# Optimization experiments

Hardware: AMD Instinct MI355X
Metric: run time of the kernel (lower is better)

Reference implementation:

```python
import jax, jax.numpy as jnp
import numpy as np

DIM = 768
TIME_DIM = 768
NUM_HEADS = 12
NUM_PATCHES = 784
GRID = 28  # sqrt(NUM_PATCHES)
REL_MAX = 2 * GRID - 1  # 55


def _rel_pos_indices():
    # Faithful to the torch buffer: relative_position_index = (dh + g-1) + (dw + g-1)
    coords = np.stack(np.meshgrid(np.arange(GRID), np.arange(GRID), indexing='ij'))  # [2,g,g]
    cf = coords.reshape(2, -1)  # [2,N]
    rel = cf[:, :, None] - cf[:, None, :]  # [2,N,N]
    rel = rel.transpose(1, 2, 0)
    rel[:, :, 0] += GRID - 1
    rel[:, :, 1] += GRID - 1
    idx = rel.sum(-1)  # [N,N], values in [0, 2*(2g-2)]
    # forward then splits this summed index (as written in the source):
    ih = idx // REL_MAX
    iw = idx % REL_MAX
    return jnp.asarray(ih, jnp.int32), jnp.asarray(iw, jnp.int32)


def setup_inputs() -> dict:
    key = jax.random.key(0)
    ks = jax.random.split(key, 16)
    B = 8
    s = 0.02
    inp = {
        'x_s': jax.random.normal(ks[0], (B, NUM_PATCHES, DIM), jnp.float32),
        'x_t': jax.random.normal(ks[1], (B, TIME_DIM), jnp.float32),
        'Wqs': jax.random.normal(ks[2], (DIM, DIM), jnp.float32) * s,
        'Wqt': jax.random.normal(ks[3], (TIME_DIM, DIM), jnp.float32) * s,
        'Wks': jax.random.normal(ks[4], (DIM, DIM), jnp.float32) * s,
        'Wkt': jax.random.normal(ks[5], (TIME_DIM, DIM), jnp.float32) * s,
        'Wvs': jax.random.normal(ks[6], (DIM, DIM), jnp.float32) * s,
        'Wvt': jax.random.normal(ks[7], (TIME_DIM, DIM), jnp.float32) * s,
        'rpb_table': jax.random.normal(ks[8], (REL_MAX, REL_MAX, NUM_HEADS), jnp.float32) * s,
        'proj_w': jax.random.normal(ks[9], (DIM, DIM), jnp.float32) * s,
        'proj_b': jnp.zeros((DIM,), jnp.float32),
    }
    return inp


def reference(x_s, x_t, Wqs, Wqt, Wks, Wkt, Wvs, Wvt, rpb_table, proj_w, proj_b):
    B, N, D = x_s.shape
    H = NUM_HEADS
    hd = D // H
    scale = hd ** -0.5

    # time-embed fused QKV: q = x_s @ Wqs + x_t @ Wqt (broadcast over tokens)
    q = x_s @ Wqs + (x_t @ Wqt)[:, None, :]
    k = x_s @ Wks + (x_t @ Wkt)[:, None, :]
    v = x_s @ Wvs + (x_t @ Wvt)[:, None, :]

    q = q.reshape(B, N, H, hd).transpose(0, 2, 1, 3)  # [B,H,N,hd]
    k = k.reshape(B, N, H, hd).transpose(0, 2, 1, 3)
    v = v.reshape(B, N, H, hd).transpose(0, 2, 1, 3)

    attn = jnp.einsum('bhnd,bhmd->bhnm', q, k) * scale  # [B,H,N,N]

    ih, iw = _rel_pos_indices()  # [N,N] each
    bias = rpb_table[ih, iw]  # [N,N,H]
    attn = attn + bias.transpose(2, 0, 1)[None]  # [1,H,N,N]

    attn = jax.nn.softmax(attn, axis=-1)
    x = jnp.einsum('bhnm,bhmd->bhnd', attn, v)
    x = x.transpose(0, 2, 1, 3).reshape(B, N, D)
    return x @ proj_w + proj_b
```

## Files before the change

kernel.cpp:

```cpp
#include <hip/hip_runtime.h>
#include <hip/hip_bf16.h>
#include <stdint.h>

#define DIM 768
#define NP  784
#define NH  12
#define HD  64
#define BATCH 8
#define MROWS (BATCH*NP)
#define MPAD 832
#define NCHUNK 32
#define KCH 24
#define L2E 1.4426950408889634f

using bf16x8 = __attribute__((ext_vector_type(8))) short;
using bf16x4 = __attribute__((ext_vector_type(4))) short;
using f32x4  = __attribute__((ext_vector_type(4))) float;

__device__ __forceinline__ short f2bf(float f) {
  union { float f; uint32_t u; } c; c.f = f;
  uint32_t u = c.u;
  u += 0x7FFFu + ((u >> 16) & 1u);
  return (short)(u >> 16);
}

__device__ __forceinline__ short bfr(float x) {
  union { __hip_bfloat16 b; short s; } u;
  u.b = __float2bfloat16(x);
  return u.s;
}

__device__ __forceinline__ void gld_lds16(const void* g, void* l) {
  __builtin_amdgcn_global_load_lds((const __attribute__((address_space(1))) uint32_t*)g,
                                   (__attribute__((address_space(3))) uint32_t*)l,
                                   16, 0, 0);
}

__global__ __launch_bounds__(256) void cvt_bf16_kernel(const float* __restrict__ src,
                                                       short* __restrict__ dst, int n8) {
  int i = blockIdx.x * 256 + threadIdx.x;
  if (i >= n8) return;
  const float4* s = (const float4*)src;
  float4 a = s[2*i], b = s[2*i+1];
  bf16x8 o;
  o[0]=f2bf(a.x); o[1]=f2bf(a.y); o[2]=f2bf(a.z); o[3]=f2bf(a.w);
  o[4]=f2bf(b.x); o[5]=f2bf(b.y); o[6]=f2bf(b.z); o[7]=f2bf(b.w);
  ((bf16x8*)dst)[i] = o;
}

__global__ __launch_bounds__(256) void wtrans_kernel(const float* __restrict__ w0,
                                                     const float* __restrict__ w1,
                                                     const float* __restrict__ w2,
                                                     const float* __restrict__ w3,
                                                     short* __restrict__ dst) {
  __shared__ float tile[32][33];
  const int z = blockIdx.z;
  const float* src = (z==0) ? w0 : (z==1) ? w1 : (z==2) ? w2 : w3;
  short* d = dst + (size_t)z * DIM * DIM;
  const int n0 = blockIdx.x*32, k0 = blockIdx.y*32;
  const int tx = threadIdx.x, ty = threadIdx.y;
#pragma unroll
  for (int i=0;i<4;i++) tile[ty+i*8][tx] = src[(size_t)(k0+ty+i*8)*DIM + n0+tx];
  __syncthreads();
#pragma unroll
  for (int i=0;i<4;i++) d[(size_t)(n0+ty+i*8)*DIM + k0+tx] = f2bf(tile[tx][ty+i*8]);
}

__global__ __launch_bounds__(256) void tvec1_kernel(const float* __restrict__ x_t,
                                                    const float* __restrict__ wq,
                                                    const float* __restrict__ wk,
                                                    const float* __restrict__ wv,
                                                    float* __restrict__ part) {
  const int z = blockIdx.x, kc = blockIdx.y;
  const float* w = (z==0) ? wq : (z==1) ? wk : wv;
  const int d = threadIdx.x;
  __shared__ float xs[BATCH][KCH];
  if (threadIdx.x < BATCH*KCH)
    xs[threadIdx.x / KCH][threadIdx.x % KCH] =
        x_t[(size_t)(threadIdx.x / KCH)*DIM + kc*KCH + threadIdx.x % KCH];
  __syncthreads();
  float a0[BATCH] = {}, a1[BATCH] = {}, a2[BATCH] = {};
#pragma unroll 4
  for (int k = 0; k < KCH; ++k) {
    const float* wr = w + (size_t)(kc*KCH + k)*DIM + d;
    float w0 = wr[0], w1 = wr[256], w2 = wr[512];
#pragma unroll
    for (int b = 0; b < BATCH; ++b) {
      float xv = xs[b][k];
      a0[b] += xv*w0; a1[b] += xv*w1; a2[b] += xv*w2;
    }
  }
#pragma unroll
  for (int b = 0; b < BATCH; ++b) {
    float* p = part + (((size_t)z*NCHUNK + kc)*BATCH + b)*DIM + d;
    p[0] = a0[b]; p[256] = a1[b]; p[512] = a2[b];
  }
}

__global__ __launch_bounds__(256) void tvec2_kernel(const float* __restrict__ part,
                                                    float* __restrict__ t) {
  const int i = blockIdx.x*256 + threadIdx.x;
  if (i >= 3*BATCH*DIM) return;
  const int z = i / (BATCH*DIM), rem = i % (BATCH*DIM);
  float s = 0.f;
#pragma unroll 8
  for (int c = 0; c < NCHUNK; ++c)
    s += part[((size_t)z*NCHUNK + c)*BATCH*DIM + rem];
  t[i] = s;
}

template<int MODE>
__global__ __launch_bounds__(256) void gemm_kernel(const short* __restrict__ A,
                                                   const short* __restrict__ Bw,
                                                   const float* __restrict__ aux,
                                                   short* __restrict__ outq,
                                                   short* __restrict__ outk,
                                                   short* __restrict__ outv,
                                                   float* __restrict__ outf) {
  __shared__ short As[128*32];
  __shared__ short Bs[128*32];
  const int bx = blockIdx.x, by = blockIdx.y, z = blockIdx.z;
  const short* Bz = Bw + (size_t)z * DIM * DIM;
  const int tid = threadIdx.x, w = tid>>6, lane = tid&63;
  const int wr = w>>1, wc = w&1, ln15 = lane&15, lg = lane>>4;
  const int m0 = by*128, n0 = bx*128;

  f32x4 acc[4][4] = {};

  for (int kt=0; kt<24; ++kt) {
    const int k0 = kt*32;
    __syncthreads();
#pragma unroll
    for (int i=0;i<2;i++) {
      const int inst = w*2 + i;
      const int off  = inst*1024 + lane*16;
      const int row  = off >> 6;
      const int ce   = (off & 63) >> 1;
      gld_lds16(A  + (size_t)(m0+row)*DIM + k0 + ce, (char*)As + (size_t)inst*1024);
      gld_lds16(Bz + (size_t)(n0+row)*DIM + k0 + ce, (char*)Bs + (size_t)inst*1024);
    }
    __syncthreads();
    bf16x8 af[4], bfr_[4];
#pragma unroll
    for (int mi=0;mi<4;mi++) af[mi]   = *(const bf16x8*)&As[(wr*64+mi*16+ln15)*32 + lg*8];
#pragma unroll
    for (int ni=0;ni<4;ni++) bfr_[ni] = *(const bf16x8*)&Bs[(wc*64+ni*16+ln15)*32 + lg*8];
#pragma unroll
    for (int mi=0;mi<4;mi++)
#pragma unroll
      for (int ni=0;ni<4;ni++)
        acc[mi][ni] = __builtin_amdgcn_mfma_f32_16x16x32_bf16(af[mi], bfr_[ni], acc[mi][ni], 0,0,0);
  }

  if (MODE == 0) {
    const float scl = (z==0) ? 0.125f * L2E : 1.0f;
#pragma unroll
    for (int mi=0;mi<4;mi++) {
#pragma unroll
      for (int j=0;j<4;j++) {
        const int r  = m0 + wr*64 + mi*16 + lg*4 + j;
        const int bb = r / NP;
        const int m  = r - bb*NP;
        const float* tv = aux + ((size_t)z*BATCH + bb) * DIM;
        if (z == 0) {
#pragma unroll
          for (int ni=0;ni<4;ni++) {
            const int gcol = n0 + wc*64 + ni*16 + ln15;
            outq[(size_t)r*DIM + gcol] = f2bf((acc[mi][ni][j] + tv[gcol]) * scl);
          }
        } else if (z == 1) {
#pragma unroll
          for (int ni=0;ni<4;ni++) {
            const int gcol = n0 + wc*64 + ni*16 + ln15;
            const int h = gcol >> 6, d = gcol & 63;
            outk[((size_t)(bb*NH + h)*MPAD + m)*HD + d] = f2bf(acc[mi][ni][j] + tv[gcol]);
          }
        }
      }
      if (MODE == 0 && z == 2) {
        const int r0 = m0 + wr*64 + mi*16 + lg*4;
        const int bb = r0 / NP;
        const int m  = r0 - bb*NP;
        const float* tv = aux + ((size_t)2*BATCH + bb) * DIM;
#pragma unroll
        for (int ni=0;ni<4;ni++) {
          const int gcol = n0 + wc*64 + ni*16 + ln15;
          const int h = gcol >> 6, d = gcol & 63;
          const float tb = tv[gcol];
          bf16x4 ov;
          ov[0] = f2bf(acc[mi][ni][0] + tb);
          ov[1] = f2bf(acc[mi][ni][1] + tb);
          ov[2] = f2bf(acc[mi][ni][2] + tb);
          ov[3] = f2bf(acc[mi][ni][3] + tb);
          *(bf16x4*)&outv[((size_t)(bb*NH + h)*HD + d)*MPAD + m] = ov;
        }
      }
    }
  } else {
#pragma unroll
    for (int mi=0;mi<4;mi++)
#pragma unroll
      for (int j=0;j<4;j++) {
        const int r = m0 + wr*64 + mi*16 + lg*4 + j;
#pragma unroll
        for (int ni=0;ni<4;ni++) {
          const int gcol = n0 + wc*64 + ni*16 + ln15;
          outf[(size_t)r*DIM + gcol] = acc[mi][ni][j] + aux[gcol];
        }
      }
  }
}

__global__ __launch_bounds__(256) void attn3_kernel(const short* __restrict__ Qb,
                                                    const short* __restrict__ Kt,
                                                    const short* __restrict__ Vt,
                                                    const float* __restrict__ rpb,
                                                    short* __restrict__ Ob) {
  __shared__ short kt[2][4096];
  __shared__ short vt[2][4096];
  __shared__ float bias_ext[112];
  const int hw = blockIdx.x;
  const int lgid = (hw & 7) * 156 + (hw >> 3);
  const int qt = lgid % 13;
  const int bh = lgid / 13;
  const int h = bh % NH, b = bh / NH;
  const int q0 = qt*64, tid = threadIdx.x, w = tid >> 6, lane = tid & 63;
  const int ln15 = lane & 15, lg = lane >> 4;

  if (tid < 109) bias_ext[tid + 2] = rpb[(tid/55)*(55*NH) + (tid%55)*NH + h] * L2E;
  if (tid == 109) { bias_ext[0] = 0.f; bias_ext[1] = 0.f; bias_ext[111] = 0.f; }

  const bool active = (q0 + w*16) < NP;
  const int q_idx = q0 + w*16 + ln15;
  bf16x8 qf0 = {}, qf1 = {};
  if (active) {
    const short* qp = Qb + ((size_t)(b*NP) + q_idx)*DIM + h*HD + lg*8;
    qf0 = *(const bf16x8*)qp;
    qf1 = *(const bf16x8*)(qp + 32);
  }
  const int qs56 = q_idx/28 + q_idx%28 + 56;

  const int lr = lane >> 3, lc = lane & 7;
  const int swe = (lc ^ lr) << 3;
  const size_t bhs = (size_t)bh;
  const short* kp0 = Kt + (bhs*MPAD + (size_t)(w*8 + lr))*HD + swe;
  const short* kp1 = kp0 + 32*HD;
  const short* vp0 = Vt + (bhs*HD + (size_t)(w*8 + lr))*MPAD + swe;
  const short* vp1 = vp0 + 32*MPAD;

#define STAGE4(BUF) { \
    char* kb_ = (char*)kt[BUF]; char* vb_ = (char*)vt[BUF]; \
    gld_lds16(kp0, kb_ + w*1024); \
    gld_lds16(kp1, kb_ + (w+4)*1024); \
    gld_lds16(vp0, vb_ + w*1024); \
    gld_lds16(vp1, vb_ + (w+4)*1024); \
    kp0 += 64*HD; kp1 += 64*HD; vp0 += 64; vp1 += 64; }

  float m_run = -3.0e38f, l_run = 0.f;
  f32x4 o0 = {}, o1 = {}, o2 = {}, o3 = {};

  STAGE4(0)

  for (int t = 0; t < 13; ++t) {
    const int cur = t & 1;
    const int m0 = t * 64;
    __syncthreads();
    if (t < 12) STAGE4(cur^1)
    if (active) {
      const char* kb = (const char*)kt[cur];
      const int sw = (ln15 & 7) << 4;
      f32x4 s[4];
#pragma unroll
      for (int mc = 0; mc < 4; ++mc) {
        const int rb = (mc*16 + ln15) * 128;
        bf16x8 kf0 = *(const bf16x8*)(kb + rb + ((lg*16) ^ sw));
        bf16x8 kf1 = *(const bf16x8*)(kb + rb + ((lg*16 + 64) ^ sw));
        f32x4 acc = {};
        acc = __builtin_amdgcn_mfma_f32_16x16x32_bf16(kf0, qf0, acc, 0,0,0);
        acc = __builtin_amdgcn_mfma_f32_16x16x32_bf16(kf1, qf1, acc, 0,0,0);
        s[mc] = acc;
      }
#pragma unroll
      for (int mc = 0; mc < 4; ++mc) {
        const int mb = m0 + mc*16 + lg*4;
        const int a28 = (mb * 2341) >> 16;
        const int idx0 = qs56 - mb + 27*a28;
        s[mc][0] += bias_ext[idx0];
        s[mc][1] += bias_ext[idx0-1];
        s[mc][2] += bias_ext[idx0-2];
        s[mc][3] += bias_ext[idx0-3];
      }
      if (m0 + 64 > NP) {
#pragma unroll
        for (int mc = 0; mc < 4; ++mc)
#pragma unroll
          for (int j = 0; j < 4; ++j)
            if (m0 + mc*16 + lg*4 + j >= NP) s[mc][j] = -1e30f;
      }
      float t0 = fmaxf(fmaxf(s[0][0],s[0][1]), fmaxf(s[0][2],s[0][3]));
      float t1 = fmaxf(fmaxf(s[1][0],s[1][1]), fmaxf(s[1][2],s[1][3]));
      float t2 = fmaxf(fmaxf(s[2][0],s[2][1]), fmaxf(s[2][2],s[2][3]));
      float t3 = fmaxf(fmaxf(s[3][0],s[3][1]), fmaxf(s[3][2],s[3][3]));
      float tm = fmaxf(fmaxf(t0,t1), fmaxf(t2,t3));
      tm = fmaxf(tm, __shfl_xor(tm, 16));
      tm = fmaxf(tm, __shfl_xor(tm, 32));
      const bool grow = !__all(tm - m_run <= 8.0f);
      float m_new = m_run, f = 1.0f;
      if (grow) { m_new = fmaxf(m_run, tm); f = exp2f(m_run - m_new); }
      float ts = 0.f;
#pragma unroll
      for (int mc = 0; mc < 4; ++mc) {
        float p0 = exp2f(s[mc][0]-m_new), p1 = exp2f(s[mc][1]-m_new);
        float p2 = exp2f(s[mc][2]-m_new), p3 = exp2f(s[mc][3]-m_new);
        s[mc][0]=p0; s[mc][1]=p1; s[mc][2]=p2; s[mc][3]=p3;
        ts += (p0+p1)+(p2+p3);
      }
      ts += __shfl_xor(ts, 16);
      ts += __shfl_xor(ts, 32);
      if (grow) {
        l_run = l_run * f + ts;
        m_run = m_new;
        o0 *= f; o1 *= f; o2 *= f; o3 *= f;
      } else {
        l_run += ts;
      }
      bf16x4 pb[4];
#pragma unroll
      for (int mc = 0; mc < 4; ++mc) {
        pb[mc][0] = bfr(s[mc][0]); pb[mc][1] = bfr(s[mc][1]);
        pb[mc][2] = bfr(s[mc][2]); pb[mc][3] = bfr(s[mc][3]);
      }
      const char* vb = (const char*)vt[cur];
#pragma unroll
      for (int mc = 0; mc < 4; ++mc) {
        const int ib = (mc*32 + lg*8) ^ sw;
        bf16x4 vf0 = *(const bf16x4*)(vb + (0*16+ln15)*128 + ib);
        bf16x4 vf1 = *(const bf16x4*)(vb + (1*16+ln15)*128 + ib);
        bf16x4 vf2 = *(const bf16x4*)(vb + (2*16+ln15)*128 + ib);
        bf16x4 vf3 = *(const bf16x4*)(vb + (3*16+ln15)*128 + ib);
        o0 = __builtin_amdgcn_mfma_f32_16x16x16bf16_1k(vf0, pb[mc], o0, 0,0,0);
        o1 = __builtin_amdgcn_mfma_f32_16x16x16bf16_1k(vf1, pb[mc], o1, 0,0,0);
        o2 = __builtin_amdgcn_mfma_f32_16x16x16bf16_1k(vf2, pb[mc], o2, 0,0,0);
        o3 = __builtin_amdgcn_mfma_f32_16x16x16bf16_1k(vf3, pb[mc], o3, 0,0,0);
      }
    }
  }
#undef STAGE4

  if (active) {
    const float inv = 1.0f / l_run;
    short* op = Ob + ((size_t)(b*NP) + q_idx)*DIM + h*HD + lg*4;
    bf16x4 ov;
    ov[0]=bfr(o0[0]*inv); ov[1]=bfr(o0[1]*inv); ov[2]=bfr(o0[2]*inv); ov[3]=bfr(o0[3]*inv);
    *(bf16x4*)(op + 0*16) = ov;
    ov[0]=bfr(o1[0]*inv); ov[1]=bfr(o1[1]*inv); ov[2]=bfr(o1[2]*inv); ov[3]=bfr(o1[3]*inv);
    *(bf16x4*)(op + 1*16) = ov;
    ov[0]=bfr(o2[0]*inv); ov[1]=bfr(o2[1]*inv); ov[2]=bfr(o2[2]*inv); ov[3]=bfr(o2[3]*inv);
    *(bf16x4*)(op + 2*16) = ov;
    ov[0]=bfr(o3[0]*inv); ov[1]=bfr(o3[1]*inv); ov[2]=bfr(o3[2]*inv); ov[3]=bfr(o3[3]*inv);
    *(bf16x4*)(op + 3*16) = ov;
  }
}

extern "C" void kernel_launch(void* const* d_in, const int* in_sizes, int n_in,
                              void* d_out, int out_size, void* d_ws, size_t ws_size,
                              hipStream_t stream) {
  const float* x_s = (const float*)d_in[0];
  const float* x_t = (const float*)d_in[1];
  const float* Wqs = (const float*)d_in[2];
  const float* Wqt = (const float*)d_in[3];
  const float* Wks = (const float*)d_in[4];
  const float* Wkt = (const float*)d_in[5];
  const float* Wvs = (const float*)d_in[6];
  const float* Wvt = (const float*)d_in[7];
  const float* rpb = (const float*)d_in[8];
  const float* pw  = (const float*)d_in[9];
  const float* pb  = (const float*)d_in[10];
  float* out = (float*)d_out;

  char* ws = (char*)d_ws;
  size_t off = 0;
  float* t_part = (float*)(ws + off); off += (size_t)3*NCHUNK*BATCH*DIM*4;
  float* t_vec  = (float*)(ws + off); off += (size_t)3*BATCH*DIM*4;
  short* Wt     = (short*)(ws + off); off += (size_t)4*DIM*DIM*2;
  short* Qb     = (short*)(ws + off); off += (size_t)MROWS*DIM*2;
  short* Ob     = (short*)(ws + off); off += (size_t)MROWS*DIM*2;
  short* Xb     = (short*)(ws + off); off += (size_t)MROWS*DIM*2;
  short* Kt     = (short*)(ws + off); off += (size_t)BATCH*NH*MPAD*HD*2;
  short* Vt     = (short*)(ws + off); off += (size_t)BATCH*NH*MPAD*HD*2;

  cvt_bf16_kernel<<<2352, 256, 0, stream>>>(x_s, Xb, MROWS*DIM/8);
  wtrans_kernel<<<dim3(24,24,4), dim3(32,8), 0, stream>>>(Wqs, Wks, Wvs, pw, Wt);
  tvec1_kernel<<<dim3(3,NCHUNK), 256, 0, stream>>>(x_t, Wqt, Wkt, Wvt, t_part);
  tvec2_kernel<<<72, 256, 0, stream>>>(t_part, t_vec);
  gemm_kernel<0><<<dim3(6,49,3), 256, 0, stream>>>(Xb, Wt, t_vec, Qb, Kt, Vt, nullptr);
  attn3_kernel<<<1248, 256, 0, stream>>>(Qb, Kt, Vt, rpb, Ob);
  gemm_kernel<1><<<dim3(6,49,1), 256, 0, stream>>>(Ob, Wt + (size_t)3*DIM*DIM, pb,
                                                   nullptr, nullptr, nullptr, out);
}
```

Measured before the change: 139.4 us.

## Widen attention blocks to 128 queries with 8 waves and vectorize bias lookup

The attention kernel now uses 512-thread blocks covering 128 query rows (7 tiles per head instead of 13). Each K/V tile staged in shared memory is therefore reused by twice as many waves, and each wave issues half as many global-to-LDS loads. The relative-position bias table is pre-expanded into float4 entries, so four shifted bias values come from one LDS read instead of four scalar reads. The risks are fewer blocks (672), more idle waves in the last query tile (only 784 of 896 rows are real), and a larger shared-memory bias table.

```diff
diff --git a/kernel.cpp b/kernel.cpp
--- a/kernel.cpp
+++ b/kernel.cpp
@@ -211,24 +211,34 @@
   }
 }
 
-__global__ __launch_bounds__(256) void attn3_kernel(const short* __restrict__ Qb,
+__global__ __launch_bounds__(512) void attn4_kernel(const short* __restrict__ Qb,
                                                     const short* __restrict__ Kt,
                                                     const short* __restrict__ Vt,
                                                     const float* __restrict__ rpb,
                                                     short* __restrict__ Ob) {
   __shared__ short kt[2][4096];
   __shared__ short vt[2][4096];
-  __shared__ float bias_ext[112];
+  __shared__ float4 bias4[112];
   const int hw = blockIdx.x;
-  const int lgid = (hw & 7) * 156 + (hw >> 3);
-  const int qt = lgid % 13;
-  const int bh = lgid / 13;
+  const int lgid = (hw & 7) * 84 + (hw >> 3);
+  const int qt = lgid % 7;
+  const int bh = lgid / 7;
   const int h = bh % NH, b = bh / NH;
-  const int q0 = qt*64, tid = threadIdx.x, w = tid >> 6, lane = tid & 63;
+  const int q0 = qt*128, tid = threadIdx.x, w = tid >> 6, lane = tid & 63;
   const int ln15 = lane & 15, lg = lane >> 4;
 
-  if (tid < 109) bias_ext[tid + 2] = rpb[(tid/55)*(55*NH) + (tid%55)*NH + h] * L2E;
-  if (tid == 109) { bias_ext[0] = 0.f; bias_ext[1] = 0.f; bias_ext[111] = 0.f; }
+  if (tid < 112) {
+    float4 v;
+#pragma unroll
+    for (int j = 0; j < 4; ++j) {
+      const int i = tid - j - 2;
+      float bv = 0.f;
+      if (i >= 0 && i < 109)
+        bv = rpb[(i/55)*(55*NH) + (i%55)*NH + h] * L2E;
+      ((float*)&v)[j] = bv;
+    }
+    bias4[tid] = v;
+  }
 
   const bool active = (q0 + w*16) < NP;
   const int q_idx = q0 + w*16 + ln15;
@@ -244,28 +254,23 @@
   const int swe = (lc ^ lr) << 3;
   const size_t bhs = (size_t)bh;
   const short* kp0 = Kt + (bhs*MPAD + (size_t)(w*8 + lr))*HD + swe;
-  const short* kp1 = kp0 + 32*HD;
   const short* vp0 = Vt + (bhs*HD + (size_t)(w*8 + lr))*MPAD + swe;
-  const short* vp1 = vp0 + 32*MPAD;
-
-#define STAGE4(BUF) { \
-    char* kb_ = (char*)kt[BUF]; char* vb_ = (char*)vt[BUF]; \
-    gld_lds16(kp0, kb_ + w*1024); \
-    gld_lds16(kp1, kb_ + (w+4)*1024); \
-    gld_lds16(vp0, vb_ + w*1024); \
-    gld_lds16(vp1, vb_ + (w+4)*1024); \
-    kp0 += 64*HD; kp1 += 64*HD; vp0 += 64; vp1 += 64; }
+
+#define STAGE2(BUF) { \
+    gld_lds16(kp0, (char*)kt[BUF] + w*1024); \
+    gld_lds16(vp0, (char*)vt[BUF] + w*1024); \
+    kp0 += 64*HD; vp0 += 64; }
 
   float m_run = -3.0e38f, l_run = 0.f;
   f32x4 o0 = {}, o1 = {}, o2 = {}, o3 = {};
 
-  STAGE4(0)
+  STAGE2(0)
 
   for (int t = 0; t < 13; ++t) {
     const int cur = t & 1;
     const int m0 = t * 64;
     __syncthreads();
-    if (t < 12) STAGE4(cur^1)
+    if (t < 12) STAGE2(cur^1)
     if (active) {
       const char* kb = (const char*)kt[cur];
       const int sw = (ln15 & 7) << 4;
@@ -285,10 +290,11 @@
         const int mb = m0 + mc*16 + lg*4;
         const int a28 = (mb * 2341) >> 16;
         const int idx0 = qs56 - mb + 27*a28;
-        s[mc][0] += bias_ext[idx0];
-        s[mc][1] += bias_ext[idx0-1];
-        s[mc][2] += bias_ext[idx0-2];
-        s[mc][3] += bias_ext[idx0-3];
+        const float4 b4 = bias4[idx0];
+        s[mc][0] += b4.x;
+        s[mc][1] += b4.y;
+        s[mc][2] += b4.z;
+        s[mc][3] += b4.w;
       }
       if (m0 + 64 > NP) {
 #pragma unroll
@@ -345,7 +351,7 @@
       }
     }
   }
-#undef STAGE4
+#undef STAGE2
 
   if (active) {
     const float inv = 1.0f / l_run;
@@ -394,7 +400,7 @@
   tvec1_kernel<<<dim3(3,NCHUNK), 256, 0, stream>>>(x_t, Wqt, Wkt, Wvt, t_part);
   tvec2_kernel<<<72, 256, 0, stream>>>(t_part, t_vec);
   gemm_kernel<0><<<dim3(6,49,3), 256, 0, stream>>>(Xb, Wt, t_vec, Qb, Kt, Vt, nullptr);
-  attn3_kernel<<<1248, 256, 0, stream>>>(Qb, Kt, Vt, rpb, Ob);
+  attn4_kernel<<<672, 512, 0, stream>>>(Qb, Kt, Vt, rpb, Ob);
   gemm_kernel<1><<<dim3(6,49,1), 256, 0, stream>>>(Ob, Wt + (size_t)3*DIM*DIM, pb,
                                                    nullptr, nullptr, nullptr, out);
 }
```

Result: faster. 134.2 us (-3.7%).
